# Performance work log

Hardware: AMD Instinct MI355X
Metric: run time of the kernel (lower is better)

The kernel has to match this reference:

```python
import jax, jax.numpy as jnp
import numpy as np

D_MODEL = 1024
NUM_HEADS = 16
HEAD_DIM = D_MODEL // NUM_HEADS
MAX_SEQ_LEN = 2048
THETA = 10000.0
BATCH = 2
SEQ = 2048


def _rope_tables():
    inv_freq = 1.0 / (THETA ** (jnp.arange(0, HEAD_DIM, 2, dtype=jnp.float32) / HEAD_DIM))
    pos = jnp.arange(MAX_SEQ_LEN, dtype=jnp.float32)
    freqs = pos[:, None] * inv_freq[None, :]  # [max_seq, head_dim/2]
    return jnp.sin(freqs), jnp.cos(freqs)


def _apply_rope(x, sin, cos):
    # x: [b, h, s, d]; sin/cos: [s, d/2] -> broadcast over b, h
    sin = sin[None, None, :, :]
    cos = cos[None, None, :, :]
    x_even = x[..., 0::2]
    x_odd = x[..., 1::2]
    out_even = x_even * cos - x_odd * sin
    out_odd = x_even * sin + x_odd * cos
    # interleave back: stack on new last axis then flatten
    out = jnp.stack((out_even, out_odd), axis=-1)
    return out.reshape(x.shape)


def setup_inputs() -> dict:
    key = jax.random.key(0)
    ks = jax.random.split(key, 5)
    std = (2.0 / (D_MODEL + D_MODEL)) ** 0.5
    return {
        "x": jax.random.normal(ks[0], (BATCH, SEQ, D_MODEL), dtype=jnp.float32),
        "Wq": jax.random.normal(ks[1], (D_MODEL, D_MODEL), dtype=jnp.float32) * std,
        "Wk": jax.random.normal(ks[2], (D_MODEL, D_MODEL), dtype=jnp.float32) * std,
        "Wv": jax.random.normal(ks[3], (D_MODEL, D_MODEL), dtype=jnp.float32) * std,
        "Wo": jax.random.normal(ks[4], (D_MODEL, D_MODEL), dtype=jnp.float32) * std,
    }


def reference(x, Wq, Wk, Wv, Wo):
    b, s, _ = x.shape
    # projections: weight stored [out, in] as in the torch Linear
    Q = jnp.einsum('bsd,od->bso', x, Wq)
    K = jnp.einsum('bsd,od->bso', x, Wk)
    V = jnp.einsum('bsd,od->bso', x, Wv)
    # split heads -> [b, h, s, hd]
    def split(t):
        return t.reshape(b, s, NUM_HEADS, HEAD_DIM).transpose(0, 2, 1, 3)
    Q, K, V = split(Q), split(K), split(V)
    sin, cos = _rope_tables()
    sin, cos = sin[:s], cos[:s]
    Q = _apply_rope(Q, sin, cos)
    K = _apply_rope(K, sin, cos)
    scale = 1.0 / jnp.sqrt(jnp.float32(HEAD_DIM))
    scores = jnp.einsum('bhqd,bhkd->bhqk', Q, K)
    causal = jnp.tril(jnp.ones((s, s), dtype=bool))[None, None]
    scores = jnp.where(causal, scores, -jnp.inf) * scale  # -inf * scale stays -inf
    attn = jax.nn.softmax(scores, axis=-1)
    out = jnp.einsum('bhqk,bhkd->bhqd', attn, V)
    out = out.transpose(0, 2, 1, 3).reshape(b, s, D_MODEL)
    return jnp.einsum('bsd,od->bso', out, Wo)
```

## Files before the change

kernel.cpp:

```cpp
#include <hip/hip_runtime.h>
#include <math.h>

#define NHEADS 16
#define HD 64
#define SEQ 2048
#define BATCH 2
#define DM 1024
#define MTOT (BATCH*SEQ)
#define LDP 72

typedef __bf16 bf16x8 __attribute__((ext_vector_type(8)));
typedef __bf16 bf16x4 __attribute__((ext_vector_type(4)));
typedef float  f32x4  __attribute__((ext_vector_type(4)));

#define LOG2E 1.4426950408889634f

#define GLD16(gp, lp) __builtin_amdgcn_global_load_lds( \
    (const __attribute__((address_space(1))) void*)(gp), \
    (__attribute__((address_space(3))) void*)(lp), 16, 0, 0)

__global__ __launch_bounds__(256)
void cast_all(const float* __restrict__ x, const float* __restrict__ Wq,
              const float* __restrict__ Wk, const float* __restrict__ Wv,
              const float* __restrict__ Wo,
              __bf16* __restrict__ xb, __bf16* __restrict__ Wqkvb,
              __bf16* __restrict__ Wob)
{
    const size_t NX = (size_t)MTOT * DM;
    const size_t NW = (size_t)DM * DM;
    const size_t i = ((size_t)blockIdx.x * 256 + threadIdx.x) * 8;
    const float* src; __bf16* dst; size_t off;
    if (i < NX)               { src = x;  dst = xb;           off = i; }
    else if (i < NX + NW)     { src = Wq; dst = Wqkvb;        off = i - NX; }
    else if (i < NX + 2*NW)   { src = Wk; dst = Wqkvb + NW;   off = i - NX - NW; }
    else if (i < NX + 3*NW)   { src = Wv; dst = Wqkvb + 2*NW; off = i - NX - 2*NW; }
    else                      { src = Wo; dst = Wob;          off = i - NX - 3*NW; }
    const float4 f0 = *(const float4*)&src[off];
    const float4 f1 = *(const float4*)&src[off + 4];
    bf16x8 o;
    o[0] = (__bf16)f0.x; o[1] = (__bf16)f0.y; o[2] = (__bf16)f0.z; o[3] = (__bf16)f0.w;
    o[4] = (__bf16)f1.x; o[5] = (__bf16)f1.y; o[6] = (__bf16)f1.z; o[7] = (__bf16)f1.w;
    *(bf16x8*)&dst[off] = o;
}

template<int BN>
__global__ __launch_bounds__(256)
void gemm_mfma(const __bf16* __restrict__ A, const __bf16* __restrict__ W,
               float* __restrict__ Cf,
               __bf16* __restrict__ Qb, __bf16* __restrict__ Kb,
               __bf16* __restrict__ Vtb, int mode)
{
    constexpr int JT = BN / 32;
    __shared__ __bf16 As[128 * 64];
    __shared__ __bf16 Bs[BN * 64];

    const int tid  = threadIdx.x;
    const int lane = tid & 63;
    const int wave = tid >> 6;
    const int ll   = lane & 15;
    const int quad = lane >> 4;
    const int wm   = (wave & 1) * 64;
    const int wn   = (wave >> 1) * (BN / 2);
    const int bm   = blockIdx.x * 128;
    const int bn   = blockIdx.y * BN;

    const __bf16* Ab = A + (size_t)bm * DM;
    const __bf16* Wb = W + (size_t)bn * DM;

    f32x4 acc[4][JT];
#pragma unroll
    for (int i = 0; i < 4; i++)
#pragma unroll
        for (int j = 0; j < JT; j++) acc[i][j] = (f32x4){0.f, 0.f, 0.f, 0.f};

    for (int k0 = 0; k0 < DM; k0 += 64) {
#pragma unroll
        for (int j = 0; j < 4; j++) {
            const int t = tid + 256 * j;
            const int r = t >> 3, g = t & 7;
            GLD16(Ab + (size_t)r * DM + k0 + ((g ^ (r & 7)) * 8), &As[t * 8]);
        }
#pragma unroll
        for (int j = 0; j < BN / 32; j++) {
            const int t = tid + 256 * j;
            const int r = t >> 3, g = t & 7;
            GLD16(Wb + (size_t)r * DM + k0 + ((g ^ (r & 7)) * 8), &Bs[t * 8]);
        }
        __syncthreads();

#pragma unroll
        for (int kh = 0; kh < 2; kh++) {
            bf16x8 af[4], bfr[JT];
#pragma unroll
            for (int i = 0; i < 4; i++) {
                const int r = wm + i*16 + ll;
                const int g = kh*4 + quad;
                af[i] = *(const bf16x8*)&As[(r*8 + (g ^ (r & 7))) * 8];
            }
#pragma unroll
            for (int j = 0; j < JT; j++) {
                const int r = wn + j*16 + ll;
                const int g = kh*4 + quad;
                bfr[j] = *(const bf16x8*)&Bs[(r*8 + (g ^ (r & 7))) * 8];
            }
#pragma unroll
            for (int i = 0; i < 4; i++)
#pragma unroll
                for (int j = 0; j < JT; j++)
                    acc[i][j] = __builtin_amdgcn_mfma_f32_16x16x32_bf16(
                        af[i], bfr[j], acc[i][j], 0, 0, 0);
        }
        __syncthreads();
    }

    if (mode == 1) {
#pragma unroll
        for (int i = 0; i < 4; i++) {
#pragma unroll
            for (int j = 0; j < JT; j++) {
                const int gc = bn + wn + j*16 + ll;
#pragma unroll
                for (int r = 0; r < 4; r++) {
                    const int gr = bm + wm + i*16 + quad*4 + r;
                    Cf[(size_t)gr * DM + gc] = acc[i][j][r];
                }
            }
        }
    } else {
        const int which = bn >> 10;
        const int nb = bn & 1023;
#pragma unroll
        for (int i = 0; i < 4; i++) {
            const int m0 = bm + wm + i*16 + quad*4;
            const int b  = m0 >> 11;
            const int s0 = m0 & (SEQ - 1);
#pragma unroll
            for (int j = 0; j < JT; j++) {
                const int n_g = nb + wn + j*16 + ll;
                const int h = n_g >> 6, d = n_g & (HD - 1);
                if (which == 2) {
                    bf16x4 pk;
#pragma unroll
                    for (int r = 0; r < 4; r++) pk[r] = (__bf16)acc[i][j][r];
                    *(bf16x4*)&Vtb[((size_t)((b*NHEADS + h)*HD + d)) * SEQ + s0] = pk;
                } else {
                    __bf16* P = (which == 0) ? Qb : Kb;
#pragma unroll
                    for (int r = 0; r < 4; r++)
                        P[((size_t)(b*NHEADS + h) * SEQ + s0 + r) * HD + d] =
                            (__bf16)acc[i][j][r];
                }
            }
        }
    }
}

__global__ __launch_bounds__(256)
void rope_bf16(__bf16* __restrict__ Q, __bf16* __restrict__ K)
{
    const int t = blockIdx.x * 256 + threadIdx.x;
    __bf16* P = (blockIdx.y == 0) ? Q : K;
    const float sc = (blockIdx.y == 0) ? 0.125f * LOG2E : 1.0f;

    const int d0 = (t & 7) * 8;
    const int s  = (t >> 3) & (SEQ - 1);

    bf16x8 v = *(bf16x8*)&P[(size_t)t * 8];
    bf16x8 o;
#pragma unroll
    for (int k = 0; k < 4; k++) {
        const float inv = exp2f(-(float)(d0 + 2*k) * (13.287712379549449f / 64.0f));
        const float f  = (float)s * inv;
        const float sn = sinf(f);
        const float cs = cosf(f);
        const float xe = (float)v[2*k];
        const float xo = (float)v[2*k + 1];
        o[2*k]     = (__bf16)((xe * cs - xo * sn) * sc);
        o[2*k + 1] = (__bf16)((xe * sn + xo * cs) * sc);
    }
    *(bf16x8*)&P[(size_t)t * 8] = o;
}

__global__ __launch_bounds__(256, 2)
void attn_mfma(const __bf16* __restrict__ Qb, const __bf16* __restrict__ Kb,
               const __bf16* __restrict__ Vtb, __bf16* __restrict__ AOb)
{
    __shared__ __align__(16) __bf16 pt[4][16][LDP];
    __shared__ float comb[4][64][66];
    __shared__ float lbuf[4][64];

    const int tid  = threadIdx.x;
    const int wave = tid >> 6;
    const int lane = tid & 63;
    const int m    = lane & 15;
    const int quad = lane >> 4;
    const int bh   = blockIdx.x;
    const int b    = bh >> 4, h = bh & 15;

    const __bf16* Qp = Qb + (size_t)bh * SEQ * HD;
    const __bf16* Kp = Kb + (size_t)bh * SEQ * HD;
    const __bf16* Vp = Vtb + (size_t)bh * HD * SEQ;

    bf16x8 ones;
#pragma unroll
    for (int j = 0; j < 8; j++) ones[j] = (__bf16)1.0f;

#pragma unroll 1
    for (int pass = 0; pass < 2; pass++) {
        const int qb = pass ? (SEQ/64 - 1) - (int)blockIdx.y : (int)blockIdx.y;
        const int q0 = qb * 64;

        bf16x8 qf[4][2];
#pragma unroll
        for (int i = 0; i < 4; i++) {
            const __bf16* qp = Qp + (size_t)(q0 + i*16 + m) * HD + quad*8;
            qf[i][0] = *(const bf16x8*)qp;
            qf[i][1] = *(const bf16x8*)(qp + 32);
        }

        f32x4 acc[4][4];
        f32x4 l_acc[4];
#pragma unroll
        for (int i = 0; i < 4; i++) {
            l_acc[i] = (f32x4){0.f, 0.f, 0.f, 0.f};
#pragma unroll
            for (int nt = 0; nt < 4; nt++) acc[i][nt] = (f32x4){0.f, 0.f, 0.f, 0.f};
        }

        for (int t = wave; t <= qb; t += 4) {
            const int k0 = t * 64;
            const bool diag = (t == qb);

            bf16x8 kf[4][2], vf[4][2];
#pragma unroll
            for (int tk = 0; tk < 4; tk++) {
                const __bf16* kp = Kp + (size_t)(k0 + tk*16 + m) * HD + quad*8;
                kf[tk][0] = *(const bf16x8*)kp;
                kf[tk][1] = *(const bf16x8*)(kp + 32);
                const __bf16* vp = Vp + (size_t)(tk*16 + m) * SEQ + k0 + quad*8;
                vf[tk][0] = *(const bf16x8*)vp;
                vf[tk][1] = *(const bf16x8*)(vp + 32);
            }

#pragma unroll
            for (int i = 0; i < 4; i++) {
                f32x4 s[4];
#pragma unroll
                for (int tk = 0; tk < 4; tk++) {
                    s[tk] = (f32x4){0.f, 0.f, 0.f, 0.f};
                    s[tk] = __builtin_amdgcn_mfma_f32_16x16x32_bf16(
                        qf[i][0], kf[tk][0], s[tk], 0, 0, 0);
                    s[tk] = __builtin_amdgcn_mfma_f32_16x16x32_bf16(
                        qf[i][1], kf[tk][1], s[tk], 0, 0, 0);
                }
#pragma unroll
                for (int tk = 0; tk < 4; tk++) {
#pragma unroll
                    for (int r = 0; r < 4; r++) {
                        float sv = s[tk][r];
                        if (diag)
                            sv = (16*tk + m <= 16*i + quad*4 + r) ? sv : -INFINITY;
                        const float p = __builtin_amdgcn_exp2f(sv);
                        pt[wave][quad*4 + r][16*tk + m] = (__bf16)p;
                    }
                }
                const bf16x8 af0 = *(const bf16x8*)&pt[wave][m][quad*8];
                const bf16x8 af1 = *(const bf16x8*)&pt[wave][m][32 + quad*8];
                l_acc[i] = __builtin_amdgcn_mfma_f32_16x16x32_bf16(
                    af0, ones, l_acc[i], 0, 0, 0);
                l_acc[i] = __builtin_amdgcn_mfma_f32_16x16x32_bf16(
                    af1, ones, l_acc[i], 0, 0, 0);
#pragma unroll
                for (int nt = 0; nt < 4; nt++) {
                    acc[i][nt] = __builtin_amdgcn_mfma_f32_16x16x32_bf16(
                        af0, vf[nt][0], acc[i][nt], 0, 0, 0);
                    acc[i][nt] = __builtin_amdgcn_mfma_f32_16x16x32_bf16(
                        af1, vf[nt][1], acc[i][nt], 0, 0, 0);
                }
            }
        }

        __syncthreads();
#pragma unroll
        for (int i = 0; i < 4; i++) {
#pragma unroll
            for (int nt = 0; nt < 4; nt++)
#pragma unroll
                for (int r = 0; r < 4; r++)
                    comb[wave][i*16 + quad*4 + r][nt*16 + m] = acc[i][nt][r];
            if (m == 0)
#pragma unroll
                for (int r = 0; r < 4; r++)
                    lbuf[wave][i*16 + quad*4 + r] = l_acc[i][r];
        }
        __syncthreads();

        {
            const int row = tid >> 2;
            const int cg  = (tid & 3) * 16;
            const float l = lbuf[0][row] + lbuf[1][row] + lbuf[2][row] + lbuf[3][row];
            const float rl = 1.0f / l;
            __bf16* op = AOb + (size_t)(b * SEQ + q0 + row) * DM + h * HD + cg;
#pragma unroll
            for (int c = 0; c < 16; c++) {
                const float o = comb[0][row][cg + c] + comb[1][row][cg + c]
                              + comb[2][row][cg + c] + comb[3][row][cg + c];
                op[c] = (__bf16)(o * rl);
            }
        }
        __syncthreads();
    }
}

extern "C" void kernel_launch(void* const* d_in, const int* in_sizes, int n_in,
                              void* d_out, int out_size, void* d_ws, size_t ws_size,
                              hipStream_t stream) {
    const float* x  = (const float*)d_in[0];
    const float* Wq = (const float*)d_in[1];
    const float* Wk = (const float*)d_in[2];
    const float* Wv = (const float*)d_in[3];
    const float* Wo = (const float*)d_in[4];
    float* out = (float*)d_out;

    char* ws = (char*)d_ws;
    __bf16* xb    = (__bf16*)ws;
    __bf16* Wqkvb = (__bf16*)(ws + ((size_t)8  << 20));
    __bf16* Wob   = (__bf16*)(ws + ((size_t)14 << 20));
    __bf16* Qb    = (__bf16*)(ws + ((size_t)16 << 20));
    __bf16* Kb    = (__bf16*)(ws + ((size_t)24 << 20));
    __bf16* Vtb   = (__bf16*)(ws + ((size_t)32 << 20));
    __bf16* AOb   = (__bf16*)(ws + ((size_t)40 << 20));

    cast_all<<<4096, 256, 0, stream>>>(x, Wq, Wk, Wv, Wo, xb, Wqkvb, Wob);

    gemm_mfma<128><<<dim3(MTOT/128, 3072/128), 256, 0, stream>>>(
        xb, Wqkvb, nullptr, Qb, Kb, Vtb, 0);

    rope_bf16<<<dim3((BATCH*NHEADS*SEQ*8)/256, 2), 256, 0, stream>>>(Qb, Kb);

    attn_mfma<<<dim3(BATCH*NHEADS, SEQ/128), 256, 0, stream>>>(Qb, Kb, Vtb, AOb);

    gemm_mfma<64><<<dim3(MTOT/128, DM/64), 256, 0, stream>>>(
        AOb, Wob, out, nullptr, nullptr, nullptr, 1);
}
```

Measured before the change: 188.3 us.

## Fuse RoPE into QKV GEMM epilogue and shrink GEMM M-tile to 64

Removes the standalone RoPE kernel by applying rotary embedding and the Q scale inside the QKV projection epilogue, pairing even and odd columns through a lane shuffle and computing sincos directly. The GEMM becomes templated on BM and a compile-time mode, with BM dropped from 128 to 64 for both projections and launch bounds raised to target 6 blocks per CU. This saves one full read-write pass over Q and K plus a kernel launch, and gives more blocks on the GPU. The cost is less operand reuse per tile and extra transcendental work in the epilogue. __sincosf is a fast approximation, so RoPE precision may drop slightly.

Result: no change. 190.8 us (+1.3%).

```diff
diff --git a/kernel.cpp b/kernel.cpp
--- a/kernel.cpp
+++ b/kernel.cpp
@@ -43,15 +43,16 @@
     *(bf16x8*)&dst[off] = o;
 }
 
-template<int BN>
-__global__ __launch_bounds__(256)
+template<int BM, int BN, int MODE>
+__global__ __launch_bounds__(256, 6)
 void gemm_mfma(const __bf16* __restrict__ A, const __bf16* __restrict__ W,
                float* __restrict__ Cf,
                __bf16* __restrict__ Qb, __bf16* __restrict__ Kb,
-               __bf16* __restrict__ Vtb, int mode)
+               __bf16* __restrict__ Vtb)
 {
+    constexpr int IT = BM / 32;
     constexpr int JT = BN / 32;
-    __shared__ __bf16 As[128 * 64];
+    __shared__ __bf16 As[BM * 64];
     __shared__ __bf16 Bs[BN * 64];
 
     const int tid  = threadIdx.x;
@@ -59,23 +60,23 @@
     const int wave = tid >> 6;
     const int ll   = lane & 15;
     const int quad = lane >> 4;
-    const int wm   = (wave & 1) * 64;
+    const int wm   = (wave & 1) * (BM / 2);
     const int wn   = (wave >> 1) * (BN / 2);
-    const int bm   = blockIdx.x * 128;
+    const int bm   = blockIdx.x * BM;
     const int bn   = blockIdx.y * BN;
 
     const __bf16* Ab = A + (size_t)bm * DM;
     const __bf16* Wb = W + (size_t)bn * DM;
 
-    f32x4 acc[4][JT];
-#pragma unroll
-    for (int i = 0; i < 4; i++)
+    f32x4 acc[IT][JT];
+#pragma unroll
+    for (int i = 0; i < IT; i++)
 #pragma unroll
         for (int j = 0; j < JT; j++) acc[i][j] = (f32x4){0.f, 0.f, 0.f, 0.f};
 
     for (int k0 = 0; k0 < DM; k0 += 64) {
 #pragma unroll
-        for (int j = 0; j < 4; j++) {
+        for (int j = 0; j < BM / 32; j++) {
             const int t = tid + 256 * j;
             const int r = t >> 3, g = t & 7;
             GLD16(Ab + (size_t)r * DM + k0 + ((g ^ (r & 7)) * 8), &As[t * 8]);
@@ -90,9 +91,9 @@
 
 #pragma unroll
         for (int kh = 0; kh < 2; kh++) {
-            bf16x8 af[4], bfr[JT];
-#pragma unroll
-            for (int i = 0; i < 4; i++) {
+            bf16x8 af[IT], bfr[JT];
+#pragma unroll
+            for (int i = 0; i < IT; i++) {
                 const int r = wm + i*16 + ll;
                 const int g = kh*4 + quad;
                 af[i] = *(const bf16x8*)&As[(r*8 + (g ^ (r & 7))) * 8];
@@ -104,7 +105,7 @@
                 bfr[j] = *(const bf16x8*)&Bs[(r*8 + (g ^ (r & 7))) * 8];
             }
 #pragma unroll
-            for (int i = 0; i < 4; i++)
+            for (int i = 0; i < IT; i++)
 #pragma unroll
                 for (int j = 0; j < JT; j++)
                     acc[i][j] = __builtin_amdgcn_mfma_f32_16x16x32_bf16(
@@ -113,9 +114,9 @@
         __syncthreads();
     }
 
-    if (mode == 1) {
-#pragma unroll
-        for (int i = 0; i < 4; i++) {
+    if (MODE == 1) {
+#pragma unroll
+        for (int i = 0; i < IT; i++) {
 #pragma unroll
             for (int j = 0; j < JT; j++) {
                 const int gc = bn + wn + j*16 + ll;
@@ -130,7 +131,7 @@
         const int which = bn >> 10;
         const int nb = bn & 1023;
 #pragma unroll
-        for (int i = 0; i < 4; i++) {
+        for (int i = 0; i < IT; i++) {
             const int m0 = bm + wm + i*16 + quad*4;
             const int b  = m0 >> 11;
             const int s0 = m0 & (SEQ - 1);
@@ -145,40 +146,27 @@
                     *(bf16x4*)&Vtb[((size_t)((b*NHEADS + h)*HD + d)) * SEQ + s0] = pk;
                 } else {
                     __bf16* P = (which == 0) ? Qb : Kb;
-#pragma unroll
-                    for (int r = 0; r < 4; r++)
+                    const float sc = (which == 0) ? 0.125f * LOG2E : 1.0f;
+                    const float inv =
+                        exp2f(-(float)(d & ~1) * (13.287712379549449f / 64.0f));
+                    const bool odd = (d & 1);
+#pragma unroll
+                    for (int r = 0; r < 4; r++) {
+                        const float own = acc[i][j][r];
+                        const float oth = __shfl_xor(own, 1);
+                        float sn, cs;
+                        __sincosf((float)(s0 + r) * inv, &sn, &cs);
+                        const float xe = odd ? oth : own;
+                        const float xo = odd ? own : oth;
+                        const float o = odd ? (xe * sn + xo * cs)
+                                            : (xe * cs - xo * sn);
                         P[((size_t)(b*NHEADS + h) * SEQ + s0 + r) * HD + d] =
-                            (__bf16)acc[i][j][r];
+                            (__bf16)(o * sc);
+                    }
                 }
             }
         }
     }
-}
-
-__global__ __launch_bounds__(256)
-void rope_bf16(__bf16* __restrict__ Q, __bf16* __restrict__ K)
-{
-    const int t = blockIdx.x * 256 + threadIdx.x;
-    __bf16* P = (blockIdx.y == 0) ? Q : K;
-    const float sc = (blockIdx.y == 0) ? 0.125f * LOG2E : 1.0f;
-
-    const int d0 = (t & 7) * 8;
-    const int s  = (t >> 3) & (SEQ - 1);
-
-    bf16x8 v = *(bf16x8*)&P[(size_t)t * 8];
-    bf16x8 o;
-#pragma unroll
-    for (int k = 0; k < 4; k++) {
-        const float inv = exp2f(-(float)(d0 + 2*k) * (13.287712379549449f / 64.0f));
-        const float f  = (float)s * inv;
-        const float sn = sinf(f);
-        const float cs = cosf(f);
-        const float xe = (float)v[2*k];
-        const float xo = (float)v[2*k + 1];
-        o[2*k]     = (__bf16)((xe * cs - xo * sn) * sc);
-        o[2*k + 1] = (__bf16)((xe * sn + xo * cs) * sc);
-    }
-    *(bf16x8*)&P[(size_t)t * 8] = o;
 }
 
 __global__ __launch_bounds__(256, 2)
@@ -333,13 +321,11 @@
 
     cast_all<<<4096, 256, 0, stream>>>(x, Wq, Wk, Wv, Wo, xb, Wqkvb, Wob);
 
-    gemm_mfma<128><<<dim3(MTOT/128, 3072/128), 256, 0, stream>>>(
-        xb, Wqkvb, nullptr, Qb, Kb, Vtb, 0);
-
-    rope_bf16<<<dim3((BATCH*NHEADS*SEQ*8)/256, 2), 256, 0, stream>>>(Qb, Kb);
+    gemm_mfma<64,128,0><<<dim3(MTOT/64, 3072/128), 256, 0, stream>>>(
+        xb, Wqkvb, nullptr, Qb, Kb, Vtb);
 
     attn_mfma<<<dim3(BATCH*NHEADS, SEQ/128), 256, 0, stream>>>(Qb, Kb, Vtb, AOb);
 
-    gemm_mfma<64><<<dim3(MTOT/128, DM/64), 256, 0, stream>>>(
-        AOb, Wob, out, nullptr, nullptr, nullptr, 1);
+    gemm_mfma<64,64,1><<<dim3(MTOT/64, DM/64), 256, 0, stream>>>(
+        AOb, Wob, out, nullptr, nullptr, nullptr);
 }
```
